# Kernel optimization log

Hardware: AMD Instinct MI355X
Metric: run time of the kernel (lower is better)

The kernel has to match this reference:

```python
import jax, jax.numpy as jnp
import numpy as np

IOU_THRESHOLD = 0.5

def cxcywh_to_xyxy(b):
    cx, cy, w, h = jnp.split(b, 4, axis=-1)
    return jnp.concatenate([cx - 0.5 * w, cy - 0.5 * h, cx + 0.5 * w, cy + 0.5 * h], axis=-1)

def batched_giou(p_xyxy, t_xyxy):
    # p_xyxy: [B, N, 4], t_xyxy: [B, T, 4] -> giou: [B, N, T]
    p = p_xyxy[:, :, None, :]  # [B, N, 1, 4]
    t = t_xyxy[:, None, :, :]  # [B, 1, T, 4]
    area_p = (p_xyxy[..., 2] - p_xyxy[..., 0]) * (p_xyxy[..., 3] - p_xyxy[..., 1])  # [B, N]
    area_t = (t_xyxy[..., 2] - t_xyxy[..., 0]) * (t_xyxy[..., 3] - t_xyxy[..., 1])  # [B, T]
    lt = jnp.maximum(p[..., :2], t[..., :2])
    rb = jnp.minimum(p[..., 2:], t[..., 2:])
    wh = jnp.clip(rb - lt, 0.0)
    inter = wh[..., 0] * wh[..., 1]  # [B, N, T]
    union = area_p[:, :, None] + area_t[:, None, :] - inter
    iou = inter / union
    # enclosing box
    lt_e = jnp.minimum(p[..., :2], t[..., :2])
    rb_e = jnp.maximum(p[..., 2:], t[..., 2:])
    wh_e = jnp.clip(rb_e - lt_e, 0.0)
    area_e = wh_e[..., 0] * wh_e[..., 1]
    return iou - (area_e - union) / area_e

def setup_inputs() -> dict:
    key = jax.random.key(0)
    k1, k2 = jax.random.split(key)
    B, N, T = 128, 900, 300
    pred_boxes = jax.random.uniform(k1, (B, N, 4), dtype=jnp.float32)
    target_boxes = jax.random.uniform(k2, (B, T, 4), dtype=jnp.float32)
    target_mask = jnp.ones((B, T), dtype=bool)
    return {"pred_boxes": pred_boxes, "target_boxes": target_boxes, "target_mask": target_mask}

def reference(pred_boxes, target_boxes, target_mask):
    # pred_boxes: [B, N, 4] cxcywh; target_boxes: [B, T, 4] cxcywh (padded)
    p_xyxy = cxcywh_to_xyxy(pred_boxes)
    t_xyxy = cxcywh_to_xyxy(target_boxes)
    giou = batched_giou(p_xyxy, t_xyxy)  # [B, N, T]
    max_iou = jnp.max(giou, axis=1)      # [B, T] best GIoU per target
    pred_idx = jnp.argmax(giou, axis=1)  # [B, T] matched query per target
    valid = target_mask & (max_iou >= IOU_THRESHOLD)  # [B, T] match kept
    return pred_idx, valid, max_iou
```

## Files before the change

### kernel.cpp

```cpp
#include <hip/hip_runtime.h>


#define BB 128
#define NN 900
#define TT 300
#define TCHUNK 64
#define TBLOCKS 5
#define NSPLIT 5
#define NPB 180
#define NPW 45
#define MARGIN 2e-5f

__device__ __forceinline__ float giou_exact(float4 pb, float4 tb) {
#pragma clang fp contract(off)
    float px0 = pb.x - 0.5f * pb.z, py0 = pb.y - 0.5f * pb.w;
    float px1 = pb.x + 0.5f * pb.z, py1 = pb.y + 0.5f * pb.w;
    float tx0 = tb.x - 0.5f * tb.z, ty0 = tb.y - 0.5f * tb.w;
    float tx1 = tb.x + 0.5f * tb.z, ty1 = tb.y + 0.5f * tb.w;
    float pa = (px1 - px0) * (py1 - py0);
    float ta = (tx1 - tx0) * (ty1 - ty0);
    float w  = fmaxf(fminf(px1, tx1) - fmaxf(px0, tx0), 0.f);
    float h  = fmaxf(fminf(py1, ty1) - fmaxf(py0, ty0), 0.f);
    float inter = w * h;
    float uni   = pa + ta - inter;
    float iou   = inter / uni;
    float ew = fmaxf(fmaxf(px1, tx1) - fminf(px0, tx0), 0.f);
    float eh = fmaxf(fmaxf(py1, ty1) - fminf(py0, ty0), 0.f);
    float ea = ew * eh;
    return iou - (ea - uni) / ea;
}

__global__ __launch_bounds__(256, 8) void matcher_scan_kernel(
    const float* __restrict__ pred,
    const float* __restrict__ tgt,
    float* __restrict__ pbest,
    float* __restrict__ psec,
    int*   __restrict__ pidx)
{
    __shared__ float4 sp[NPB];
    __shared__ float  spa[NPB];
    __shared__ float  rbv[256], rsv[256];
    __shared__ int    riv[256];

    const int ns  = blockIdx.x % NSPLIT;
    const int tc  = (blockIdx.x / NSPLIT) % TBLOCKS;
    const int b   = blockIdx.x / (NSPLIT * TBLOCKS);
    const int tid = threadIdx.x;
    const int tl  = tid & 63;
    const int ng  = tid >> 6;
    const int t   = tc * TCHUNK + tl;

    if (tid < NPB) {
        const float4 pb = ((const float4*)pred)[b * NN + ns * NPB + tid];
        float4 q;
        q.x = pb.x - 0.5f * pb.z;
        q.y = pb.y - 0.5f * pb.w;
        q.z = pb.x + 0.5f * pb.z;
        q.w = pb.y + 0.5f * pb.w;
        sp[tid]  = q;
        spa[tid] = (q.z - q.x) * (q.w - q.y);
    }
    __syncthreads();

    float tx0 = 0.f, ty0 = 0.f, tx1 = 0.f, ty1 = 0.f, ta = 0.f;
    if (t < TT) {
        const float4 tb = ((const float4*)tgt)[b * TT + t];
        tx0 = tb.x - 0.5f * tb.z;
        ty0 = tb.y - 0.5f * tb.w;
        tx1 = tb.x + 0.5f * tb.z;
        ty1 = tb.y + 0.5f * tb.w;
        ta  = (tx1 - tx0) * (ty1 - ty0);
    }

    float best = -INFINITY, second = -INFINITY;
    int   bidxl = 0;
    const int k0 = ng * NPW;
    #pragma unroll 9
    for (int k = 0; k < NPW; ++k) {
        const float4 p = sp[k0 + k];
        const float pa = spa[k0 + k];

        const float w   = fmaxf(fminf(p.z, tx1) - fmaxf(p.x, tx0), 0.f);
        const float h   = fmaxf(fminf(p.w, ty1) - fmaxf(p.y, ty0), 0.f);
        const float inter = w * h;
        const float uni   = pa + ta - inter;

        const float ew = fmaxf(p.z, tx1) - fminf(p.x, tx0);
        const float eh = fmaxf(p.w, ty1) - fminf(p.y, ty0);
        const float ea = ew * eh;

        const float num = fmaf(inter, ea, uni * (uni - ea));
        const float g   = num * __builtin_amdgcn_rcpf(uni * ea);

        second = __builtin_amdgcn_fmed3f(g, best, second);
        if (g > best) bidxl = k;
        best = fmaxf(best, g);
    }
    int bidx = k0 + bidxl;

    rbv[tid] = best; rsv[tid] = second; riv[tid] = bidx;
    __syncthreads();

    if (ng == 0 && t < TT) {
        for (int s = 1; s < 4; ++s) {
            const float ob = rbv[s * 64 + tl];
            const float os = rsv[s * 64 + tl];
            const int   oi = riv[s * 64 + tl];
            second = fmaxf(fminf(best, ob), fmaxf(second, os));
            if (ob > best) { best = ob; bidx = oi; }
        }
        const int bt = b * TT + t;
        pbest[ns * BB * TT + bt] = best;
        psec [ns * BB * TT + bt] = second;
        pidx [ns * BB * TT + bt] = ns * NPB + bidx;
    }
}

__global__ __launch_bounds__(256) void matcher_finish_kernel(
    const float* __restrict__ pbest,
    const float* __restrict__ psec,
    const int*   __restrict__ pidx,
    const float* __restrict__ pred,
    const float* __restrict__ tgt,
    const unsigned char* __restrict__ mask,
    float* __restrict__ out)
{
    __shared__ int sflag[256];
    __shared__ int scount;

    const int tid = threadIdx.x;
    const int bt  = blockIdx.x * 256 + tid;
    if (tid == 0) scount = 0;
    __syncthreads();

    float best = -INFINITY, second = -INFINITY;
    int   bidx = 0;
    #pragma unroll
    for (int s = 0; s < NSPLIT; ++s) {
        const float ob = pbest[s * BB * TT + bt];
        const float os = psec [s * BB * TT + bt];
        const int   oi = pidx [s * BB * TT + bt];
        second = fmaxf(fminf(best, ob), fmaxf(second, os));
        if (ob > best) { best = ob; bidx = oi; }
    }

    if (best - second > MARGIN) {
        const int b = bt / TT;
        const float4 pb = ((const float4*)pred)[b * NN + bidx];
        const float4 tb = ((const float4*)tgt)[bt];
        const float g = giou_exact(pb, tb);
        const bool valid = (mask[bt] != 0) && (g >= 0.5f);
        out[bt]               = (float)bidx;
        out[BB * TT + bt]     = valid ? 1.f : 0.f;
        out[2 * BB * TT + bt] = g;
    } else {
        const int pos = atomicAdd(&scount, 1);
        sflag[pos] = tid;
    }
    __syncthreads();

    const int cnt  = scount;
    const int lane = tid & 63;
    const int ng   = tid >> 6;
    for (int f = ng; f < cnt; f += 4) {
        const int fbt = blockIdx.x * 256 + sflag[f];
        const int b   = fbt / TT;
        const float4 tb = ((const float4*)tgt)[fbt];

        float bestx = -INFINITY;
        int   bix   = NN;
        for (int n = lane; n < NN; n += 64) {
            const float4 pb = ((const float4*)pred)[b * NN + n];
            const float g = giou_exact(pb, tb);
            if (g > bestx) { bestx = g; bix = n; }
        }
        for (int off = 32; off >= 1; off >>= 1) {
            const float ob = __shfl_xor(bestx, off);
            const int   oi = __shfl_xor(bix, off);
            if (ob > bestx || (ob == bestx && oi < bix)) { bestx = ob; bix = oi; }
        }
        if (lane == 0) {
            const bool valid = (mask[fbt] != 0) && (bestx >= 0.5f);
            out[fbt]               = (float)bix;
            out[BB * TT + fbt]     = valid ? 1.f : 0.f;
            out[2 * BB * TT + fbt] = bestx;
        }
    }
}

extern "C" void kernel_launch(void* const* d_in, const int* in_sizes, int n_in,
                              void* d_out, int out_size, void* d_ws, size_t ws_size,
                              hipStream_t stream) {
    const float* pred = (const float*)d_in[0];
    const float* tgt  = (const float*)d_in[1];
    const unsigned char* mask = (const unsigned char*)d_in[2];
    float* out = (float*)d_out;

    const size_t seg = (size_t)NSPLIT * BB * TT * 4;
    char* ws = (char*)d_ws;
    float* pbest = (float*)ws;
    float* psec  = (float*)(ws + seg);
    int*   pidx  = (int*)  (ws + 2 * seg);

    matcher_scan_kernel<<<dim3(BB * TBLOCKS * NSPLIT), dim3(256), 0, stream>>>(
        pred, tgt, pbest, psec, pidx);
    matcher_finish_kernel<<<dim3(BB * TT / 256), dim3(256), 0, stream>>>(
        pbest, psec, pidx, pred, tgt, mask, out);
}
```

Baseline: 93.76 us.

## Precompute pred corners and sizes in prep kernel; derive enclosing box algebraically

Adds a prep kernel that converts predictions to xyxy and stores area, width and height in a 32-byte record in workspace. The scan kernel now reads these records straight from global memory, so the shared-memory staging and its barrier go away. The enclosing width and height come from (pw+tw) minus the intersection extent, which saves two min/max operations per pair. In exchange it adds a kernel launch, doubles global read traffic per prediction, and changes rounding slightly; the margin check and exact recompute in the finish kernel are meant to absorb that.

```diff
diff --git a/kernel.cpp b/kernel.cpp
--- a/kernel.cpp
+++ b/kernel.cpp
@@ -30,17 +30,38 @@
     return iou - (ea - uni) / ea;
 }
 
+__global__ __launch_bounds__(256) void matcher_prep_kernel(
+    const float4* __restrict__ pred,
+    float4* __restrict__ pxy)
+{
+    const int i = blockIdx.x * 256 + threadIdx.x;
+    if (i >= BB * NN) return;
+    const float4 pb = pred[i];
+    float4 q;
+    q.x = pb.x - 0.5f * pb.z;
+    q.y = pb.y - 0.5f * pb.w;
+    q.z = pb.x + 0.5f * pb.z;
+    q.w = pb.y + 0.5f * pb.w;
+    const float pw = q.z - q.x;
+    const float ph = q.w - q.y;
+    float4 c;
+    c.x = pw * ph;
+    c.y = pw;
+    c.z = ph;
+    c.w = 0.f;
+    pxy[2 * i]     = q;
+    pxy[2 * i + 1] = c;
+}
+
 __global__ __launch_bounds__(256, 8) void matcher_scan_kernel(
-    const float* __restrict__ pred,
+    const float4* __restrict__ pxy,
     const float* __restrict__ tgt,
     float* __restrict__ pbest,
     float* __restrict__ psec,
     int*   __restrict__ pidx)
 {
-    __shared__ float4 sp[NPB];
-    __shared__ float  spa[NPB];
-    __shared__ float  rbv[256], rsv[256];
-    __shared__ int    riv[256];
+    __shared__ float rbv[256], rsv[256];
+    __shared__ int   riv[256];
 
     const int ns  = blockIdx.x % NSPLIT;
     const int tc  = (blockIdx.x / NSPLIT) % TBLOCKS;
@@ -50,43 +71,42 @@
     const int ng  = tid >> 6;
     const int t   = tc * TCHUNK + tl;
 
-    if (tid < NPB) {
-        const float4 pb = ((const float4*)pred)[b * NN + ns * NPB + tid];
-        float4 q;
-        q.x = pb.x - 0.5f * pb.z;
-        q.y = pb.y - 0.5f * pb.w;
-        q.z = pb.x + 0.5f * pb.z;
-        q.w = pb.y + 0.5f * pb.w;
-        sp[tid]  = q;
-        spa[tid] = (q.z - q.x) * (q.w - q.y);
-    }
-    __syncthreads();
-
-    float tx0 = 0.f, ty0 = 0.f, tx1 = 0.f, ty1 = 0.f, ta = 0.f;
+    float tx0 = 0.f, ty0 = 0.f, tx1 = 0.f, ty1 = 0.f;
+    float ta = 0.f, tw = 0.f, th = 0.f;
     if (t < TT) {
         const float4 tb = ((const float4*)tgt)[b * TT + t];
         tx0 = tb.x - 0.5f * tb.z;
         ty0 = tb.y - 0.5f * tb.w;
         tx1 = tb.x + 0.5f * tb.z;
         ty1 = tb.y + 0.5f * tb.w;
-        ta  = (tx1 - tx0) * (ty1 - ty0);
-    }
+        tw = tx1 - tx0;
+        th = ty1 - ty0;
+        ta = tw * th;
+    }
+
+    const int k0 = ng * NPW;
+    const float4* pp = pxy + 2 * (b * NN + ns * NPB + k0);
 
     float best = -INFINITY, second = -INFINITY;
     int   bidxl = 0;
-    const int k0 = ng * NPW;
-    #pragma unroll 9
+    #pragma unroll 5
     for (int k = 0; k < NPW; ++k) {
-        const float4 p = sp[k0 + k];
-        const float pa = spa[k0 + k];
-
-        const float w   = fmaxf(fminf(p.z, tx1) - fmaxf(p.x, tx0), 0.f);
-        const float h   = fmaxf(fminf(p.w, ty1) - fmaxf(p.y, ty0), 0.f);
+        const float4 q = pp[2 * k];
+        const float4 c = pp[2 * k + 1];
+
+        const float m1x = fminf(q.z, tx1);
+        const float M0x = fmaxf(q.x, tx0);
+        const float wr  = m1x - M0x;
+        const float w   = fmaxf(wr, 0.f);
+        const float m1y = fminf(q.w, ty1);
+        const float M0y = fmaxf(q.y, ty0);
+        const float hr  = m1y - M0y;
+        const float h   = fmaxf(hr, 0.f);
         const float inter = w * h;
-        const float uni   = pa + ta - inter;
-
-        const float ew = fmaxf(p.z, tx1) - fminf(p.x, tx0);
-        const float eh = fmaxf(p.w, ty1) - fminf(p.y, ty0);
+        const float uni   = (c.x + ta) - inter;
+
+        const float ew = (c.y + tw) - wr;
+        const float eh = (c.z + th) - hr;
         const float ea = ew * eh;
 
         const float num = fmaf(inter, ea, uni * (uni - ea));
@@ -198,12 +218,15 @@
 
     const size_t seg = (size_t)NSPLIT * BB * TT * 4;
     char* ws = (char*)d_ws;
-    float* pbest = (float*)ws;
-    float* psec  = (float*)(ws + seg);
-    int*   pidx  = (int*)  (ws + 2 * seg);
-
+    float*  pbest = (float*)ws;
+    float*  psec  = (float*)(ws + seg);
+    int*    pidx  = (int*)  (ws + 2 * seg);
+    float4* pxy   = (float4*)(ws + 3 * seg);
+
+    matcher_prep_kernel<<<dim3((BB * NN + 255) / 256), dim3(256), 0, stream>>>(
+        (const float4*)pred, pxy);
     matcher_scan_kernel<<<dim3(BB * TBLOCKS * NSPLIT), dim3(256), 0, stream>>>(
-        pred, tgt, pbest, psec, pidx);
+        pxy, tgt, pbest, psec, pidx);
     matcher_finish_kernel<<<dim3(BB * TT / 256), dim3(256), 0, stream>>>(
         pbest, psec, pidx, pred, tgt, mask, out);
 }
```

New measurement: 124.1 us. +32.3%, slower.
